# Optimization experiments

Hardware: AMD Instinct MI355X
Metric: run time of the kernel (lower is better)

The kernel has to match this reference:

```python
import jax, jax.numpy as jnp
import numpy as np

B, T_ENC, D_IN = 64, 32, 4096
T_DEC, D_WORD = 20, 300
H = 512
VOCAB = 20000


def lstm_scan(x_tbd, W, b, c0, h0):
    """TF BasicLSTMCell (forget_bias=1.0, gate order i,j,f,o) scanned over time.
    x_tbd: [T,B,D]; W: [D+H, 4H]; returns (c,h) final state and all h [T,B,H]."""
    def step(carry, x):
        c, h = carry
        z = jnp.concatenate([x, h], axis=-1) @ W + b  # [B,4H]
        i, j, f, o = jnp.split(z, 4, axis=-1)
        c = c * jax.nn.sigmoid(f + 1.0) + jax.nn.sigmoid(i) * jnp.tanh(j)
        h = jnp.tanh(c) * jax.nn.sigmoid(o)
        return (c, h), h
    (c, h), hs = jax.lax.scan(step, (c0, h0), x_tbd)
    return (c, h), hs


def setup_inputs() -> dict:
    key = jax.random.key(0)
    ks = jax.random.split(key, 8)
    frames = jax.random.normal(ks[0], (B, T_ENC, D_IN), dtype=jnp.float32)
    caption = jax.random.randint(ks[1], (B, T_DEC), 0, VOCAB, dtype=jnp.int32)
    embeddings = jax.random.normal(ks[2], (VOCAB, D_WORD), dtype=jnp.float32) * 0.1
    s_enc = 1.0 / np.sqrt(D_IN + H)
    s_dec = 1.0 / np.sqrt(D_WORD + H)
    W_enc = jax.random.normal(ks[3], (D_IN + H, 4 * H), dtype=jnp.float32) * s_enc
    b_enc = jnp.zeros((4 * H,), dtype=jnp.float32)
    W_dec = jax.random.normal(ks[4], (D_WORD + H, 4 * H), dtype=jnp.float32) * s_dec
    b_dec = jnp.zeros((4 * H,), dtype=jnp.float32)
    W_proj = jax.random.normal(ks[5], (H, D_WORD), dtype=jnp.float32) / np.sqrt(H)
    b_proj = jnp.zeros((D_WORD,), dtype=jnp.float32)
    return {"frames": frames, "embeddings": embeddings, "W_enc": W_enc,
            "b_enc": b_enc, "W_dec": W_dec, "b_dec": b_dec,
            "W_proj": W_proj, "b_proj": b_proj, "caption": caption}


def reference(frames, embeddings, W_enc, b_enc, W_dec, b_dec, W_proj, b_proj, caption):
    b = frames.shape[0]
    c0 = jnp.zeros((b, H), dtype=frames.dtype)
    h0 = jnp.zeros((b, H), dtype=frames.dtype)
    # encoder over frames (dropout keep_prob=1 -> identity)
    (c, h), _ = lstm_scan(jnp.swapaxes(frames, 0, 1), W_enc, b_enc, c0, h0)
    # teacher-forced decoder over caption embeddings
    cap_emb = embeddings[caption]                      # [B,T_dec,D_word]
    _, hs = lstm_scan(jnp.swapaxes(cap_emb, 0, 1), W_dec, b_dec, c, h)  # [T,B,H]
    # per-step shared dense hidden->word, vectorized over time
    word_vecs = hs @ W_proj + b_proj                   # [T,B,D_word]
    return jnp.swapaxes(word_vecs, 0, 1)               # [B,T_dec,D_word]
```

## Files before the change

kernel.cpp:

```cpp
#include <hip/hip_runtime.h>
#include <hip/hip_bf16.h>

#define BATCH  64
#define T_ENC  32
#define D_IN   4096
#define T_DEC  20
#define D_WORD 300
#define HID    512
#define FOURH  2048
#define NWG    64
#define FPAD   32
#define ZP     13

typedef __attribute__((ext_vector_type(8))) short short8;
typedef __attribute__((ext_vector_type(4))) float f32x4;
typedef unsigned long long ull;

static __device__ __forceinline__ unsigned short f2bf(float f){
  union { float f; unsigned u; } v; v.f = f;
  unsigned r = v.u + 0x7fffu + ((v.u >> 16) & 1u);
  return (unsigned short)(r >> 16);
}
static __device__ __forceinline__ float bf2f(unsigned short b){
  union { unsigned u; float f; } v; v.u = ((unsigned)b) << 16;
  return v.f;
}
static __device__ __forceinline__ float sigm(float x){
  return __builtin_amdgcn_rcpf(1.f + __expf(-x));
}
static __device__ __forceinline__ float tanh_f(float x){
  float e = __expf(2.f * x);
  return 1.f - 2.f * __builtin_amdgcn_rcpf(e + 1.f);
}

__global__ __launch_bounds__(256) void prep(
    const float* __restrict__ frames, const float* __restrict__ W_enc,
    unsigned short* __restrict__ fb, unsigned short* __restrict__ wt,
    unsigned* __restrict__ flags)
{
  const int g = blockIdx.x * 256 + threadIdx.x;
  if (blockIdx.x == 0){
    for (int i = threadIdx.x; i < NWG * FPAD; i += 256)
      __hip_atomic_store(&flags[i], 0u, __ATOMIC_RELAXED, __HIP_MEMORY_SCOPE_AGENT);
  }
  if (g < 1048576){
    const long base = (long)g * 8;
    float4 x0 = *(const float4*)(frames + base);
    float4 x1 = *(const float4*)(frames + base + 4);
    short8 v;
    v[0] = (short)f2bf(x0.x); v[1] = (short)f2bf(x0.y);
    v[2] = (short)f2bf(x0.z); v[3] = (short)f2bf(x0.w);
    v[4] = (short)f2bf(x1.x); v[5] = (short)f2bf(x1.y);
    v[6] = (short)f2bf(x1.z); v[7] = (short)f2bf(x1.w);
    *(short8*)(fb + base) = v;
  } else {
    const int r  = g - 1048576;
    const int k0 = (r >> 11) << 3;
    const int c  = r & 2047;
    short8 v;
#pragma unroll
    for (int j = 0; j < 8; ++j)
      v[j] = (short)f2bf(W_enc[(long)(k0 + j) * FOURH + c]);
    *(short8*)&wt[(long)c * D_IN + k0] = v;
  }
}

__device__ __forceinline__ void enc_tile(
    int bx, int by, const unsigned short* __restrict__ A0,
    const unsigned short* __restrict__ Wt, const float* __restrict__ bias,
    float* __restrict__ Z, char* smem)
{
  char* As = smem;
  char* Bs = smem + 16384;
  const int tid = threadIdx.x;
  const int row0 = bx * 128, col0 = by * 128;

  const int ar = tid >> 1, ah = tid & 1;
  long asrc;
  {
    int R = row0 + ar;
    int b = R & 63, t = R >> 6;
    asrc = (long)(b * T_ENC + t) * D_IN;
  }
  const int bc = tid & 127, bh = tid >> 7;
  const long bsrc = (long)(col0 + bc) * D_IN;

  const int wave = tid >> 6, lane = tid & 63;
  const int wm = (wave >> 1) * 64, wn = (wave & 1) * 64;
  const int lr = lane & 15, lkb = (lane >> 4) << 4, lq = (lane >> 4) << 2;

  f32x4 acc[4][4];
#pragma unroll
  for (int m = 0; m < 4; ++m)
#pragma unroll
    for (int n = 0; n < 4; ++n) acc[m][n] = (f32x4){0.f, 0.f, 0.f, 0.f};

#define ELOAD(DA, DB, IT) do { \
    const long ka = (long)(IT) * 64 + ah * 32; \
    const long kb = (long)(IT) * 64 + bh * 32; \
    _Pragma("unroll") \
    for (int j = 0; j < 4; ++j){ \
      DA[j] = *(const short8*)(A0 + asrc + ka + j * 8); \
      DB[j] = *(const short8*)(Wt + bsrc + kb + j * 8); \
    } \
  } while (0)

  short8 aR[4], bR[4];
  ELOAD(aR, bR, 0);

  for (int it = 0; it < 64; ++it){
    __syncthreads();
#pragma unroll
    for (int j = 0; j < 4; ++j){
      *(short8*)(As + ar * 128 + ((ah * 64 + j * 16) ^ ((ar & 7) << 4))) = aR[j];
      *(short8*)(Bs + bc * 128 + ((bh * 64 + j * 16) ^ ((bc & 7) << 4))) = bR[j];
    }
    __syncthreads();
    short8 aN[4], bN[4];
    ELOAD(aN, bN, (it + 1) & 63);
#pragma unroll
    for (int kk = 0; kk < 2; ++kk){
      short8 af[4], bfv[4];
#pragma unroll
      for (int m = 0; m < 4; ++m){
        const int r = wm + m * 16 + lr;
        af[m] = *(const short8*)(As + r * 128 + ((kk * 64 + lkb) ^ ((r & 7) << 4)));
      }
#pragma unroll
      for (int n = 0; n < 4; ++n){
        const int r = wn + n * 16 + lr;
        bfv[n] = *(const short8*)(Bs + r * 128 + ((kk * 64 + lkb) ^ ((r & 7) << 4)));
      }
#pragma unroll
      for (int m = 0; m < 4; ++m)
#pragma unroll
        for (int n = 0; n < 4; ++n)
          acc[m][n] = __builtin_amdgcn_mfma_f32_16x16x32_bf16(af[m], bfv[n], acc[m][n], 0, 0, 0);
    }
#pragma unroll
    for (int j = 0; j < 4; ++j){ aR[j] = aN[j]; bR[j] = bN[j]; }
  }

  float b4[4];
#pragma unroll
  for (int n = 0; n < 4; ++n) b4[n] = bias[col0 + wn + n * 16 + lr];
#pragma unroll
  for (int m = 0; m < 4; ++m)
#pragma unroll
    for (int n = 0; n < 4; ++n)
#pragma unroll
      for (int r = 0; r < 4; ++r){
        int gr = row0 + wm + m * 16 + lq + r;
        int gc = col0 + wn + n * 16 + lr;
        Z[(long)gr * FOURH + gc] = acc[m][n][r] + b4[n];
      }
}

__device__ __forceinline__ void dec_tile(
    int bx, int by, const float* __restrict__ emb, const int* __restrict__ cap,
    const float* __restrict__ W, const float* __restrict__ bias,
    float* __restrict__ Z, char* smem)
{
  constexpr int KLIM  = D_WORD;
  constexpr int ITERS = (KLIM + 31) / 32;
  short* As = (short*)smem;
  short* Bs = (short*)(smem + 10240);
  const int tid = threadIdx.x;
  const int row0 = bx * 128, col0 = by * 128;

  const int ar = tid >> 1, akq = (tid & 1) * 16;
  long asrc;
  {
    int R = row0 + ar;
    int b = R & 63, t = R >> 6;
    asrc = (long)cap[b * T_DEC + t] * D_WORD;
  }
  const int bc = tid & 127, bkq = (tid >> 7) * 16;

  const int wave = tid >> 6, lane = tid & 63;
  const int wm = (wave >> 1) * 64, wn = (wave & 1) * 64;
  const int lr = lane & 15, lk = (lane >> 4) << 3, lq = (lane >> 4) << 2;

  f32x4 acc[4][4];
#pragma unroll
  for (int m = 0; m < 4; ++m)
#pragma unroll
    for (int n = 0; n < 4; ++n) acc[m][n] = (f32x4){0.f, 0.f, 0.f, 0.f};

  for (int it = 0; it < ITERS; ++it){
    const int k0 = it * 32;
    float av[16], bv[16];
#pragma unroll
    for (int i = 0; i < 16; ++i){
      int k = k0 + akq + i;
      av[i] = (k < KLIM) ? emb[asrc + k] : 0.f;
    }
#pragma unroll
    for (int i = 0; i < 16; ++i){
      int k = k0 + bkq + i;
      bv[i] = (k < KLIM) ? W[(long)k * FOURH + col0 + bc] : 0.f;
    }
    __syncthreads();
    short8 a_lo, a_hi, b_lo, b_hi;
#pragma unroll
    for (int i = 0; i < 8; ++i){
      a_lo[i] = (short)f2bf(av[i]);  a_hi[i] = (short)f2bf(av[8 + i]);
      b_lo[i] = (short)f2bf(bv[i]);  b_hi[i] = (short)f2bf(bv[8 + i]);
    }
    *(short8*)&As[ar * 40 + akq]     = a_lo;
    *(short8*)&As[ar * 40 + akq + 8] = a_hi;
    *(short8*)&Bs[bc * 40 + bkq]     = b_lo;
    *(short8*)&Bs[bc * 40 + bkq + 8] = b_hi;
    __syncthreads();
    short8 af[4], bfv[4];
#pragma unroll
    for (int m = 0; m < 4; ++m) af[m]  = *(const short8*)&As[(wm + m * 16 + lr) * 40 + lk];
#pragma unroll
    for (int n = 0; n < 4; ++n) bfv[n] = *(const short8*)&Bs[(wn + n * 16 + lr) * 40 + lk];
#pragma unroll
    for (int m = 0; m < 4; ++m)
#pragma unroll
      for (int n = 0; n < 4; ++n)
        acc[m][n] = __builtin_amdgcn_mfma_f32_16x16x32_bf16(af[m], bfv[n], acc[m][n], 0, 0, 0);
  }

  float b4[4];
#pragma unroll
  for (int n = 0; n < 4; ++n) b4[n] = bias[col0 + wn + n * 16 + lr];
#pragma unroll
  for (int m = 0; m < 4; ++m)
#pragma unroll
    for (int n = 0; n < 4; ++n)
#pragma unroll
      for (int r = 0; r < 4; ++r){
        int gr = row0 + wm + m * 16 + lq + r;
        int gc = col0 + wn + n * 16 + lr;
        Z[(long)gr * FOURH + gc] = acc[m][n][r] + b4[n];
      }
}

__global__ __launch_bounds__(256) void gemm_all(
    const unsigned short* __restrict__ fbf, const unsigned short* __restrict__ wbf,
    const float* __restrict__ b_enc, float* __restrict__ Xe,
    const float* __restrict__ emb, const int* __restrict__ cap,
    const float* __restrict__ W_dec, const float* __restrict__ b_dec,
    float* __restrict__ Xd)
{
  __shared__ __align__(16) char smem[32768];
  const int bid = blockIdx.x;
  if (bid < 256)
    enc_tile(bid >> 4, bid & 15, fbf, wbf, b_enc, Xe, smem);
  else {
    const int d = bid - 256;
    dec_tile(d >> 4, d & 15, emb, cap, W_dec, b_dec, Xd, smem);
  }
}

#define REC_GEMM(WREG) do { \
  _Pragma("unroll") \
  for (int kk = 0; kk < 8; ++kk){ \
    const int row = mh * 16 + lr; \
    short8 af = *(const short8*)(hlds + row * 1024 + \
                ((kh * 512 + kk * 64 + lkb) ^ ((row & 7) << 4))); \
    _Pragma("unroll") \
    for (int n = 0; n < 2; ++n) \
      acc[n] = __builtin_amdgcn_mfma_f32_16x16x32_bf16(af, WREG[kk][n], acc[n], 0, 0, 0); \
  } \
} while (0)

__global__ __launch_bounds__(512, 1) void lstm_seq(
    const float* __restrict__ Xe, const float* __restrict__ Xd,
    const float* __restrict__ Wre, const float* __restrict__ Wrd,
    unsigned* __restrict__ hbuf_u,
    unsigned* __restrict__ hsd_u,
    unsigned* __restrict__ flags)
{
  __shared__ __align__(16) char  hlds[64 * 1024];
  __shared__ __align__(16) float zlds[2 * 4 * 64 * ZP];
  const int tid = threadIdx.x, wgid = blockIdx.x;
  const int wave = tid >> 6, lane = tid & 63;
  const int kh = wave >> 2, mh = wave & 3;
  const int lr = lane & 15, lk = (lane >> 4) << 3;
  const int lkb = (lane >> 4) << 4, lq = (lane >> 4) << 2;

  int ocol[2];
#pragma unroll
  for (int n = 0; n < 2; ++n)
    ocol[n] = (n * 2 + (lr >> 3)) * 512 + wgid * 8 + (lr & 7);

  short8 we[8][2], wd[8][2];
#pragma unroll
  for (int kk = 0; kk < 8; ++kk)
#pragma unroll
    for (int n = 0; n < 2; ++n){
      short8 e, d;
#pragma unroll
      for (int j = 0; j < 8; ++j){
        int k = kh * 256 + kk * 32 + lk + j;
        e[j] = (short)f2bf(Wre[(long)k * FOURH + ocol[n]]);
        d[j] = (short)f2bf(Wrd[(long)k * FOURH + ocol[n]]);
      }
      we[kk][n] = e; wd[kk][n] = d;
    }

  const int cb_ = tid >> 3, cu = tid & 7;
  float c_reg = 0.f;

  if (tid < 128)
    __hip_atomic_store((ull*)hbuf_u + ((tid >> 1) * 128 + wgid * 2 + (tid & 1)), 0ull,
                       __ATOMIC_RELAXED, __HIP_MEMORY_SCOPE_AGENT);
  __syncthreads();
  if (tid == 0)
    __hip_atomic_store(&flags[wgid * FPAD], 1u,
                       __ATOMIC_RELAXED, __HIP_MEMORY_SCOPE_AGENT);

  const bool mine = (lane != wgid);

  for (int q = 0; q < T_ENC + T_DEC; ++q){
    const bool dec = (q >= T_ENC);
    const int tt = dec ? q - T_ENC : q;
    const float* __restrict__ X = dec ? Xd : Xe;

    const long xb = (long)(tt * BATCH + cb_) * FOURH + wgid * 8 + cu;
    float xi = X[xb];
    float xj = X[xb + 512];
    float xf = X[xb + 1024];
    float xo = X[xb + 1536];

    {
      const unsigned tgt = (unsigned)(q + 1);
      for (;;){
        unsigned f = tgt;
        if (mine) f = __hip_atomic_load(&flags[lane * FPAD],
                                        __ATOMIC_RELAXED, __HIP_MEMORY_SCOPE_AGENT);
        if (__all((int)(f >= tgt))) break;
        __builtin_amdgcn_s_sleep(1);
      }
    }
    __builtin_amdgcn_sched_barrier(0);

    const ull* rb8 = (const ull*)(hbuf_u + (q & 1) * (BATCH * HID / 2));
    ull hv[16];
#pragma unroll
    for (int j = 0; j < 16; ++j)
      hv[j] = __hip_atomic_load(rb8 + tid + j * 512,
                                __ATOMIC_RELAXED, __HIP_MEMORY_SCOPE_AGENT);
#pragma unroll
    for (int j = 0; j < 16; ++j){
      int idx8 = tid + j * 512;
      int row = idx8 >> 7, cbb = (idx8 & 127) << 3;
      *(ull*)(hlds + row * 1024 + (cbb ^ ((row & 7) << 4))) = hv[j];
    }
    __syncthreads();

    f32x4 acc[2];
#pragma unroll
    for (int n = 0; n < 2; ++n) acc[n] = (f32x4){0.f, 0.f, 0.f, 0.f};
    if (!dec) REC_GEMM(we); else REC_GEMM(wd);

#pragma unroll
    for (int n = 0; n < 2; ++n){
      const int g = n * 2 + (lr >> 3), u = lr & 7;
#pragma unroll
      for (int r = 0; r < 4; ++r){
        const int row = mh * 16 + lq + r;
        zlds[((kh * 4 + g) * 64 + row) * ZP + u] = acc[n][r];
      }
    }
    __syncthreads();

    const int zb = cb_ * ZP + cu;
    float zi = zlds[(0 * 64) * ZP + zb] + zlds[(4 * 64) * ZP + zb] + xi;
    float zj = zlds[(1 * 64) * ZP + zb] + zlds[(5 * 64) * ZP + zb] + xj;
    float zf = zlds[(2 * 64) * ZP + zb] + zlds[(6 * 64) * ZP + zb] + xf;
    float zo = zlds[(3 * 64) * ZP + zb] + zlds[(7 * 64) * ZP + zb] + xo;
    c_reg = c_reg * sigm(zf + 1.f) + sigm(zi) * tanh_f(zj);
    float hn = tanh_f(c_reg) * sigm(zo);
    unsigned short hb = f2bf(hn);

    unsigned short* wb = (unsigned short*)(hbuf_u + ((q + 1) & 1) * (BATCH * HID / 2));
    __hip_atomic_store(&wb[cb_ * 512 + wgid * 8 + cu], hb,
                       __ATOMIC_RELAXED, __HIP_MEMORY_SCOPE_AGENT);
    if (dec)
      ((unsigned short*)hsd_u)[(tt * BATCH + cb_) * 512 + wgid * 8 + cu] = hb;

    __syncthreads();
    if (tid == 0)
      __hip_atomic_store(&flags[wgid * FPAD], (unsigned)(q + 2),
                         __ATOMIC_RELAXED, __HIP_MEMORY_SCOPE_AGENT);
  }
}

__global__ __launch_bounds__(320) void proj_kernel(
    const unsigned short* __restrict__ hsd, const float* __restrict__ Wp,
    const float* __restrict__ bp, float* __restrict__ out)
{
  __shared__ float hl[16 * 512];
  const int tid = threadIdx.x;
  const int r0 = blockIdx.x * 16;
  for (int idx = tid; idx < 16 * 512; idx += 320)
    hl[idx] = bf2f(hsd[(long)r0 * 512 + idx]);
  __syncthreads();
  if (tid < D_WORD){
    const int d = tid;
    float acc[16];
#pragma unroll
    for (int r = 0; r < 16; ++r) acc[r] = bp[d];
    for (int k = 0; k < 512; ++k){
      float w = Wp[k * D_WORD + d];
#pragma unroll
      for (int r = 0; r < 16; ++r) acc[r] += hl[r * 512 + k] * w;
    }
#pragma unroll
    for (int r = 0; r < 16; ++r){
      int R = r0 + r;
      int t = R >> 6, b = R & 63;
      out[(long)(b * T_DEC + t) * D_WORD + d] = acc[r];
    }
  }
}

extern "C" void kernel_launch(void* const* d_in, const int* in_sizes, int n_in,
                              void* d_out, int out_size, void* d_ws, size_t ws_size,
                              hipStream_t stream)
{
  const float* frames  = (const float*)d_in[0];
  const float* emb     = (const float*)d_in[1];
  const float* W_enc   = (const float*)d_in[2];
  const float* b_enc   = (const float*)d_in[3];
  const float* W_dec   = (const float*)d_in[4];
  const float* b_dec   = (const float*)d_in[5];
  const float* W_proj  = (const float*)d_in[6];
  const float* b_proj  = (const float*)d_in[7];
  const int*   caption = (const int*)d_in[8];

  char* ws = (char*)d_ws;
  float*          Xe    = (float*)(ws + 0);
  float*          Xd    = (float*)(ws + 16777216);
  unsigned*       hbuf  = (unsigned*)(ws + 27262976);
  unsigned*       hsd   = (unsigned*)(ws + 27394048);
  unsigned*       flags = (unsigned*)(ws + 28704768);
  unsigned short* fbf   = (unsigned short*)(ws + 28712960);
  unsigned short* wbf   = (unsigned short*)(ws + 45490176);
  float* out = (float*)d_out;

  prep<<<8192, 256, 0, stream>>>(frames, W_enc, fbf, wbf, flags);
  gemm_all<<<416, 256, 0, stream>>>(fbf, wbf, b_enc, Xe, emb, caption, W_dec, b_dec, Xd);
  lstm_seq<<<NWG, 512, 0, stream>>>(Xe, Xd,
                                    W_enc + (long)D_IN * FOURH,
                                    W_dec + (long)D_WORD * FOURH,
                                    hbuf, hsd, flags);
  proj_kernel<<<80, 320, 0, stream>>>((const unsigned short*)hsd, W_proj, b_proj, out);
}
```

Before: 356.5 us.

## Fuse input GEMMs into recurrent LSTM kernel with flag-driven per-timestep dataflow

Merges the separate input-projection GEMM kernel and the sequential LSTM kernel into one launch. The first 64 workgroups run the recurrence and spin on per-timestep-pair counters. The remaining workgroups compute encoder tiles, split four ways along K and accumulated with float atomics into a zeroed Xe, plus decoder tiles. This lets the recurrence start before all input projections finish, hiding GEMM time behind the serial chain. Bias addition moves into the recurrence, and Xe is zeroed in the prep kernel. The cost is atomic-add traffic, extra spin-waits, and reliance on the recurrent workgroups being co-resident to avoid deadlock.

```diff
diff --git a/kernel.cpp b/kernel.cpp
--- a/kernel.cpp
+++ b/kernel.cpp
@@ -36,12 +36,16 @@
 __global__ __launch_bounds__(256) void prep(
     const float* __restrict__ frames, const float* __restrict__ W_enc,
     unsigned short* __restrict__ fb, unsigned short* __restrict__ wt,
-    unsigned* __restrict__ flags)
+    unsigned* __restrict__ flags, float* __restrict__ Xe)
 {
   const int g = blockIdx.x * 256 + threadIdx.x;
   if (blockIdx.x == 0){
     for (int i = threadIdx.x; i < NWG * FPAD; i += 256)
       __hip_atomic_store(&flags[i], 0u, __ATOMIC_RELAXED, __HIP_MEMORY_SCOPE_AGENT);
+  }
+  {
+    float2 z2; z2.x = 0.f; z2.y = 0.f;
+    *(float2*)(Xe + (long)g * 2) = z2;
   }
   if (g < 1048576){
     const long base = (long)g * 8;
@@ -65,17 +69,17 @@
   }
 }
 
-__device__ __forceinline__ void enc_tile(
-    int bx, int by, const unsigned short* __restrict__ A0,
-    const unsigned short* __restrict__ Wt, const float* __restrict__ bias,
-    float* __restrict__ Z, char* smem)
+__device__ __forceinline__ void enc_tile8(
+    int bx, int by, int kc,
+    const unsigned short* __restrict__ A0, const unsigned short* __restrict__ Wt,
+    float* Z, char* smem, unsigned* flags)
 {
   char* As = smem;
   char* Bs = smem + 16384;
   const int tid = threadIdx.x;
   const int row0 = bx * 128, col0 = by * 128;
 
-  const int ar = tid >> 1, ah = tid & 1;
+  const int ar = tid >> 2, ah = tid & 3;
   long asrc;
   {
     int R = row0 + ar;
@@ -84,82 +88,84 @@
   }
   const int bc = tid & 127, bh = tid >> 7;
   const long bsrc = (long)(col0 + bc) * D_IN;
+  const long kbase = (long)kc * 1024;
 
   const int wave = tid >> 6, lane = tid & 63;
-  const int wm = (wave >> 1) * 64, wn = (wave & 1) * 64;
+  const int wm = (wave >> 2) * 64, wn = (wave & 3) * 32;
   const int lr = lane & 15, lkb = (lane >> 4) << 4, lq = (lane >> 4) << 2;
 
-  f32x4 acc[4][4];
+  f32x4 acc[4][2];
 #pragma unroll
   for (int m = 0; m < 4; ++m)
 #pragma unroll
-    for (int n = 0; n < 4; ++n) acc[m][n] = (f32x4){0.f, 0.f, 0.f, 0.f};
-
-#define ELOAD(DA, DB, IT) do { \
-    const long ka = (long)(IT) * 64 + ah * 32; \
-    const long kb = (long)(IT) * 64 + bh * 32; \
+    for (int n = 0; n < 2; ++n) acc[m][n] = (f32x4){0.f, 0.f, 0.f, 0.f};
+
+#define ELOAD8(DA, DB, IT) do { \
+    const long ka = kbase + (long)(IT) * 64 + ah * 16; \
+    const long kb = kbase + (long)(IT) * 64 + bh * 16; \
     _Pragma("unroll") \
-    for (int j = 0; j < 4; ++j){ \
+    for (int j = 0; j < 2; ++j){ \
       DA[j] = *(const short8*)(A0 + asrc + ka + j * 8); \
       DB[j] = *(const short8*)(Wt + bsrc + kb + j * 8); \
     } \
   } while (0)
 
-  short8 aR[4], bR[4];
-  ELOAD(aR, bR, 0);
-
-  for (int it = 0; it < 64; ++it){
-    __syncthreads();
-#pragma unroll
-    for (int j = 0; j < 4; ++j){
-      *(short8*)(As + ar * 128 + ((ah * 64 + j * 16) ^ ((ar & 7) << 4))) = aR[j];
-      *(short8*)(Bs + bc * 128 + ((bh * 64 + j * 16) ^ ((bc & 7) << 4))) = bR[j];
-    }
-    __syncthreads();
-    short8 aN[4], bN[4];
-    ELOAD(aN, bN, (it + 1) & 63);
+  short8 aR[2], bR[2];
+  ELOAD8(aR, bR, 0);
+
+  for (int it = 0; it < 16; ++it){
+    __syncthreads();
+#pragma unroll
+    for (int j = 0; j < 2; ++j){
+      *(short8*)(As + ar * 128 + ((ah * 32 + j * 16) ^ ((ar & 7) << 4))) = aR[j];
+      *(short8*)(Bs + bc * 128 + ((bh * 32 + j * 16) ^ ((bc & 7) << 4))) = bR[j];
+    }
+    __syncthreads();
+    short8 aN[2], bN[2];
+    ELOAD8(aN, bN, (it + 1) & 15);
 #pragma unroll
     for (int kk = 0; kk < 2; ++kk){
-      short8 af[4], bfv[4];
+      short8 af[4], bfv[2];
 #pragma unroll
       for (int m = 0; m < 4; ++m){
         const int r = wm + m * 16 + lr;
         af[m] = *(const short8*)(As + r * 128 + ((kk * 64 + lkb) ^ ((r & 7) << 4)));
       }
 #pragma unroll
-      for (int n = 0; n < 4; ++n){
+      for (int n = 0; n < 2; ++n){
         const int r = wn + n * 16 + lr;
         bfv[n] = *(const short8*)(Bs + r * 128 + ((kk * 64 + lkb) ^ ((r & 7) << 4)));
       }
 #pragma unroll
       for (int m = 0; m < 4; ++m)
 #pragma unroll
-        for (int n = 0; n < 4; ++n)
+        for (int n = 0; n < 2; ++n)
           acc[m][n] = __builtin_amdgcn_mfma_f32_16x16x32_bf16(af[m], bfv[n], acc[m][n], 0, 0, 0);
     }
-#pragma unroll
-    for (int j = 0; j < 4; ++j){ aR[j] = aN[j]; bR[j] = bN[j]; }
-  }
-
-  float b4[4];
-#pragma unroll
-  for (int n = 0; n < 4; ++n) b4[n] = bias[col0 + wn + n * 16 + lr];
+    aR[0] = aN[0]; aR[1] = aN[1]; bR[0] = bN[0]; bR[1] = bN[1];
+  }
+#undef ELOAD8
+
 #pragma unroll
   for (int m = 0; m < 4; ++m)
 #pragma unroll
-    for (int n = 0; n < 4; ++n)
+    for (int n = 0; n < 2; ++n)
 #pragma unroll
       for (int r = 0; r < 4; ++r){
         int gr = row0 + wm + m * 16 + lq + r;
         int gc = col0 + wn + n * 16 + lr;
-        Z[(long)gr * FOURH + gc] = acc[m][n][r] + b4[n];
-      }
-}
-
-__device__ __forceinline__ void dec_tile(
+        __hip_atomic_fetch_add(&Z[(long)gr * FOURH + gc], acc[m][n][r],
+                               __ATOMIC_RELAXED, __HIP_MEMORY_SCOPE_AGENT);
+      }
+  __syncthreads();
+  if (tid == 0)
+    __hip_atomic_fetch_add(&flags[bx * FPAD + 16], 1u,
+                           __ATOMIC_RELAXED, __HIP_MEMORY_SCOPE_AGENT);
+}
+
+__device__ __forceinline__ void dec_tile8(
     int bx, int by, const float* __restrict__ emb, const int* __restrict__ cap,
-    const float* __restrict__ W, const float* __restrict__ bias,
-    float* __restrict__ Z, char* smem)
+    const float* __restrict__ W, float* Z, char* smem, unsigned* flags)
 {
   constexpr int KLIM  = D_WORD;
   constexpr int ITERS = (KLIM + 31) / 32;
@@ -168,92 +174,74 @@
   const int tid = threadIdx.x;
   const int row0 = bx * 128, col0 = by * 128;
 
-  const int ar = tid >> 1, akq = (tid & 1) * 16;
+  const int ar = tid >> 2, akq = (tid & 3) * 8;
   long asrc;
   {
     int R = row0 + ar;
     int b = R & 63, t = R >> 6;
     asrc = (long)cap[b * T_DEC + t] * D_WORD;
   }
-  const int bc = tid & 127, bkq = (tid >> 7) * 16;
+  const int bc = tid & 127, bkq = (tid >> 7) * 8;
 
   const int wave = tid >> 6, lane = tid & 63;
-  const int wm = (wave >> 1) * 64, wn = (wave & 1) * 64;
+  const int wm = (wave >> 2) * 64, wn = (wave & 3) * 32;
   const int lr = lane & 15, lk = (lane >> 4) << 3, lq = (lane >> 4) << 2;
 
-  f32x4 acc[4][4];
+  f32x4 acc[4][2];
 #pragma unroll
   for (int m = 0; m < 4; ++m)
 #pragma unroll
-    for (int n = 0; n < 4; ++n) acc[m][n] = (f32x4){0.f, 0.f, 0.f, 0.f};
+    for (int n = 0; n < 2; ++n) acc[m][n] = (f32x4){0.f, 0.f, 0.f, 0.f};
 
   for (int it = 0; it < ITERS; ++it){
     const int k0 = it * 32;
-    float av[16], bv[16];
-#pragma unroll
-    for (int i = 0; i < 16; ++i){
+    float av[8], bv[8];
+#pragma unroll
+    for (int i = 0; i < 8; ++i){
       int k = k0 + akq + i;
       av[i] = (k < KLIM) ? emb[asrc + k] : 0.f;
     }
 #pragma unroll
-    for (int i = 0; i < 16; ++i){
+    for (int i = 0; i < 8; ++i){
       int k = k0 + bkq + i;
       bv[i] = (k < KLIM) ? W[(long)k * FOURH + col0 + bc] : 0.f;
     }
     __syncthreads();
-    short8 a_lo, a_hi, b_lo, b_hi;
+    short8 a8, b8;
 #pragma unroll
     for (int i = 0; i < 8; ++i){
-      a_lo[i] = (short)f2bf(av[i]);  a_hi[i] = (short)f2bf(av[8 + i]);
-      b_lo[i] = (short)f2bf(bv[i]);  b_hi[i] = (short)f2bf(bv[8 + i]);
-    }
-    *(short8*)&As[ar * 40 + akq]     = a_lo;
-    *(short8*)&As[ar * 40 + akq + 8] = a_hi;
-    *(short8*)&Bs[bc * 40 + bkq]     = b_lo;
-    *(short8*)&Bs[bc * 40 + bkq + 8] = b_hi;
-    __syncthreads();
-    short8 af[4], bfv[4];
+      a8[i] = (short)f2bf(av[i]);  b8[i] = (short)f2bf(bv[i]);
+    }
+    *(short8*)&As[ar * 40 + akq] = a8;
+    *(short8*)&Bs[bc * 40 + bkq] = b8;
+    __syncthreads();
+    short8 af[4], bfv[2];
 #pragma unroll
     for (int m = 0; m < 4; ++m) af[m]  = *(const short8*)&As[(wm + m * 16 + lr) * 40 + lk];
 #pragma unroll
-    for (int n = 0; n < 4; ++n) bfv[n] = *(const short8*)&Bs[(wn + n * 16 + lr) * 40 + lk];
+    for (int n = 0; n < 2; ++n) bfv[n] = *(const short8*)&Bs[(wn + n * 16 + lr) * 40 + lk];
 #pragma unroll
     for (int m = 0; m < 4; ++m)
 #pragma unroll
-      for (int n = 0; n < 4; ++n)
+      for (int n = 0; n < 2; ++n)
         acc[m][n] = __builtin_amdgcn_mfma_f32_16x16x32_bf16(af[m], bfv[n], acc[m][n], 0, 0, 0);
   }
 
-  float b4[4];
-#pragma unroll
-  for (int n = 0; n < 4; ++n) b4[n] = bias[col0 + wn + n * 16 + lr];
 #pragma unroll
   for (int m = 0; m < 4; ++m)
 #pragma unroll
-    for (int n = 0; n < 4; ++n)
+    for (int n = 0; n < 2; ++n)
 #pragma unroll
       for (int r = 0; r < 4; ++r){
         int gr = row0 + wm + m * 16 + lq + r;
         int gc = col0 + wn + n * 16 + lr;
-        Z[(long)gr * FOURH + gc] = acc[m][n][r] + b4[n];
-      }
-}
-
-__global__ __launch_bounds__(256) void gemm_all(
-    const unsigned short* __restrict__ fbf, const unsigned short* __restrict__ wbf,
-    const float* __restrict__ b_enc, float* __restrict__ Xe,
-    const float* __restrict__ emb, const int* __restrict__ cap,
-    const float* __restrict__ W_dec, const float* __restrict__ b_dec,
-    float* __restrict__ Xd)
-{
-  __shared__ __align__(16) char smem[32768];
-  const int bid = blockIdx.x;
-  if (bid < 256)
-    enc_tile(bid >> 4, bid & 15, fbf, wbf, b_enc, Xe, smem);
-  else {
-    const int d = bid - 256;
-    dec_tile(d >> 4, d & 15, emb, cap, W_dec, b_dec, Xd, smem);
-  }
+        __hip_atomic_store(&Z[(long)gr * FOURH + gc], acc[m][n][r],
+                           __ATOMIC_RELAXED, __HIP_MEMORY_SCOPE_AGENT);
+      }
+  __syncthreads();
+  if (tid == 0)
+    __hip_atomic_fetch_add(&flags[(16 + bx) * FPAD + 16], 1u,
+                           __ATOMIC_RELAXED, __HIP_MEMORY_SCOPE_AGENT);
 }
 
 #define REC_GEMM(WREG) do { \
@@ -268,16 +256,29 @@
   } \
 } while (0)
 
-__global__ __launch_bounds__(512, 1) void lstm_seq(
-    const float* __restrict__ Xe, const float* __restrict__ Xd,
+__global__ __launch_bounds__(512, 1) void fused(
+    const unsigned short* __restrict__ fbf, const unsigned short* __restrict__ wbf,
+    float* Xe,
+    const float* __restrict__ emb, const int* __restrict__ cap,
+    const float* __restrict__ W_dec, float* Xd,
     const float* __restrict__ Wre, const float* __restrict__ Wrd,
-    unsigned* __restrict__ hbuf_u,
-    unsigned* __restrict__ hsd_u,
-    unsigned* __restrict__ flags)
-{
-  __shared__ __align__(16) char  hlds[64 * 1024];
-  __shared__ __align__(16) float zlds[2 * 4 * 64 * ZP];
-  const int tid = threadIdx.x, wgid = blockIdx.x;
+    const float* __restrict__ b_enc, const float* __restrict__ b_dec,
+    unsigned* hbuf_u, unsigned* hsd_u, unsigned* flags)
+{
+  __shared__ __align__(16) char smem[65536];
+  const int bid = blockIdx.x;
+
+  if (bid >= 64){
+    int g = bid - 64;
+    if (g < 512)       enc_tile8(g >> 6, g & 15, (g >> 4) & 3, fbf, wbf, Xe, smem, flags);
+    else if (g < 672){ int d = g - 512; dec_tile8(d >> 4, d & 15, emb, cap, W_dec, Xd, smem, flags); }
+    else             { int e = g - 672; enc_tile8(8 + (e >> 6), e & 15, (e >> 4) & 3, fbf, wbf, Xe, smem, flags); }
+    return;
+  }
+
+  char*  hlds = smem;
+  float* zlds = (float*)smem;
+  const int tid = threadIdx.x, wgid = bid;
   const int wave = tid >> 6, lane = tid & 63;
   const int kh = wave >> 2, mh = wave & 3;
   const int lr = lane & 15, lk = (lane >> 4) << 3;
@@ -305,6 +306,13 @@
 
   const int cb_ = tid >> 3, cu = tid & 7;
   float c_reg = 0.f;
+
+  float be4[4], bd4[4];
+#pragma unroll
+  for (int gg = 0; gg < 4; ++gg){
+    be4[gg] = b_enc[gg * 512 + wgid * 8 + cu];
+    bd4[gg] = b_dec[gg * 512 + wgid * 8 + cu];
+  }
 
   if (tid < 128)
     __hip_atomic_store((ull*)hbuf_u + ((tid >> 1) * 128 + wgid * 2 + (tid & 1)), 0ull,
@@ -319,13 +327,22 @@
   for (int q = 0; q < T_ENC + T_DEC; ++q){
     const bool dec = (q >= T_ENC);
     const int tt = dec ? q - T_ENC : q;
-    const float* __restrict__ X = dec ? Xd : Xe;
+    float* Xp = dec ? Xd : Xe;
+
+    {
+      unsigned* xc = dec ? &flags[(16 + (tt >> 1)) * FPAD + 16]
+                         : &flags[(tt >> 1) * FPAD + 16];
+      const unsigned xtgt = dec ? 16u : 64u;
+      while (__hip_atomic_load(xc, __ATOMIC_RELAXED, __HIP_MEMORY_SCOPE_AGENT) < xtgt)
+        __builtin_amdgcn_s_sleep(2);
+    }
+    __builtin_amdgcn_sched_barrier(0);
 
     const long xb = (long)(tt * BATCH + cb_) * FOURH + wgid * 8 + cu;
-    float xi = X[xb];
-    float xj = X[xb + 512];
-    float xf = X[xb + 1024];
-    float xo = X[xb + 1536];
+    float xi = __hip_atomic_load(&Xp[xb],        __ATOMIC_RELAXED, __HIP_MEMORY_SCOPE_AGENT);
+    float xj = __hip_atomic_load(&Xp[xb +  512], __ATOMIC_RELAXED, __HIP_MEMORY_SCOPE_AGENT);
+    float xf = __hip_atomic_load(&Xp[xb + 1024], __ATOMIC_RELAXED, __HIP_MEMORY_SCOPE_AGENT);
+    float xo = __hip_atomic_load(&Xp[xb + 1536], __ATOMIC_RELAXED, __HIP_MEMORY_SCOPE_AGENT);
 
     {
       const unsigned tgt = (unsigned)(q + 1);
@@ -358,6 +375,8 @@
     for (int n = 0; n < 2; ++n) acc[n] = (f32x4){0.f, 0.f, 0.f, 0.f};
     if (!dec) REC_GEMM(we); else REC_GEMM(wd);
 
+    __syncthreads();
+
 #pragma unroll
     for (int n = 0; n < 2; ++n){
       const int g = n * 2 + (lr >> 3), u = lr & 7;
@@ -370,10 +389,10 @@
     __syncthreads();
 
     const int zb = cb_ * ZP + cu;
-    float zi = zlds[(0 * 64) * ZP + zb] + zlds[(4 * 64) * ZP + zb] + xi;
-    float zj = zlds[(1 * 64) * ZP + zb] + zlds[(5 * 64) * ZP + zb] + xj;
-    float zf = zlds[(2 * 64) * ZP + zb] + zlds[(6 * 64) * ZP + zb] + xf;
-    float zo = zlds[(3 * 64) * ZP + zb] + zlds[(7 * 64) * ZP + zb] + xo;
+    float zi = zlds[(0 * 64) * ZP + zb] + zlds[(4 * 64) * ZP + zb] + xi + (dec ? bd4[0] : be4[0]);
+    float zj = zlds[(1 * 64) * ZP + zb] + zlds[(5 * 64) * ZP + zb] + xj + (dec ? bd4[1] : be4[1]);
+    float zf = zlds[(2 * 64) * ZP + zb] + zlds[(6 * 64) * ZP + zb] + xf + (dec ? bd4[2] : be4[2]);
+    float zo = zlds[(3 * 64) * ZP + zb] + zlds[(7 * 64) * ZP + zb] + xo + (dec ? bd4[3] : be4[3]);
     c_reg = c_reg * sigm(zf + 1.f) + sigm(zi) * tanh_f(zj);
     float hn = tanh_f(c_reg) * sigm(zo);
     unsigned short hb = f2bf(hn);
@@ -444,11 +463,11 @@
   unsigned short* wbf   = (unsigned short*)(ws + 45490176);
   float* out = (float*)d_out;
 
-  prep<<<8192, 256, 0, stream>>>(frames, W_enc, fbf, wbf, flags);
-  gemm_all<<<416, 256, 0, stream>>>(fbf, wbf, b_enc, Xe, emb, caption, W_dec, b_dec, Xd);
-  lstm_seq<<<NWG, 512, 0, stream>>>(Xe, Xd,
-                                    W_enc + (long)D_IN * FOURH,
-                                    W_dec + (long)D_WORD * FOURH,
-                                    hbuf, hsd, flags);
+  prep<<<8192, 256, 0, stream>>>(frames, W_enc, fbf, wbf, flags, Xe);
+  fused<<<64 + 512 + 160 + 512, 512, 0, stream>>>(
+      fbf, wbf, Xe, emb, caption, W_dec, Xd,
+      W_enc + (long)D_IN * FOURH,
+      W_dec + (long)D_WORD * FOURH,
+      b_enc, b_dec, hbuf, hsd, flags);
   proj_kernel<<<80, 320, 0, stream>>>((const unsigned short*)hsd, W_proj, b_proj, out);
 }
```

After: 323.0 us. -9.4%, faster.
